# Optimization experiments

Measured on AMD Instinct MI355X. Metric: run time of the kernel, lower is better.

## Reference

```python
import jax, jax.numpy as jnp
import numpy as np

N, E, IN_DIM, HID, EMB, HEADS, B = 50000, 800000, 32, 128, 64, 4, 8
C = HID // HEADS
NEG_SLOPE = 0.2
LN_EPS = 1e-5
L = 3


def setup_inputs() -> dict:
    key = jax.random.key(0)
    ks = jax.random.split(key, 24)
    s = 0.05
    inp = {
        'x': jax.random.normal(ks[0], (N, IN_DIM), jnp.float32),
        'edge_index': jax.random.randint(ks[1], (2, E), 0, N),
        'edge_attr': jax.random.normal(ks[2], (E, 1), jnp.float32),
        'batch': jnp.sort(jax.random.randint(ks[3], (N,), 0, B)),
        'W_in': jax.random.normal(ks[4], (IN_DIM, HID), jnp.float32) * s,
        'b_in': jnp.zeros((HID,), jnp.float32),
        'Wl': jax.random.normal(ks[5], (L, HID, HID), jnp.float32) * s,
        'bl': jnp.zeros((L, HID), jnp.float32),
        'Wr': jax.random.normal(ks[6], (L, HID, HID), jnp.float32) * s,
        'br': jnp.zeros((L, HID), jnp.float32),
        'We': jax.random.normal(ks[7], (L, 1, HID), jnp.float32) * s,
        'att': jax.random.normal(ks[8], (L, HEADS, C), jnp.float32) * s,
        'bc': jnp.zeros((L, HID), jnp.float32),
        'ln_g': jnp.ones((L, HID), jnp.float32),
        'ln_b': jnp.zeros((L, HID), jnp.float32),
        'Wn': jax.random.normal(ks[9], (HID, EMB), jnp.float32) * s,
        'bn': jnp.zeros((EMB,), jnp.float32),
        'Wg1': jax.random.normal(ks[10], (HID, HID), jnp.float32) * s,
        'bg1': jnp.zeros((HID,), jnp.float32),
        'Wg2': jax.random.normal(ks[11], (HID, EMB), jnp.float32) * s,
        'bg2': jnp.zeros((EMB,), jnp.float32),
    }
    return inp


def _layernorm(x, g, b):
    mu = jnp.mean(x, axis=-1, keepdims=True)
    var = jnp.mean((x - mu) ** 2, axis=-1, keepdims=True)
    return (x - mu) * jax.lax.rsqrt(var + LN_EPS) * g + b


def reference(x, edge_index, edge_attr, batch, W_in, b_in, Wl, bl, Wr, br, We, att,
              bc, ln_g, ln_b, Wn, bn, Wg1, bg1, Wg2, bg2):
    src0, dst0 = edge_index[0], edge_index[1]
    # add self-loops; self-loop edge_attr = mean of incoming edge_attr (PyG fill_value='mean')
    ones = jnp.ones((E,), x.dtype)
    cnt = jax.ops.segment_sum(ones, dst0, num_segments=N)  # (N,)
    ea_self = jax.ops.segment_sum(edge_attr, dst0, num_segments=N) / jnp.maximum(cnt, 1.0)[:, None]
    ar = jnp.arange(N)
    src = jnp.concatenate([src0, ar])
    dst = jnp.concatenate([dst0, ar])
    ea = jnp.concatenate([edge_attr, ea_self], axis=0)  # (E+N, 1)

    h = x @ W_in + b_in  # (N, HID)
    for l in range(L):
        xl = (h @ Wl[l] + bl[l]).reshape(N, HEADS, C)   # source transform
        xr = (h @ Wr[l] + br[l]).reshape(N, HEADS, C)   # target transform
        ee = (ea @ We[l]).reshape(-1, HEADS, C)         # edge transform
        m = xl[src] + xr[dst] + ee                      # (E+N, H, C)
        m = jnp.where(m > 0, m, NEG_SLOPE * m)          # leaky_relu
        alpha = jnp.einsum('ehc,hc->eh', m, att[l])     # (E+N, H)
        amax = jax.ops.segment_max(alpha, dst, num_segments=N)
        ex = jnp.exp(alpha - amax[dst])
        den = jax.ops.segment_sum(ex, dst, num_segments=N)
        a = ex / den[dst]
        out = jax.ops.segment_sum(a[:, :, None] * xl[src], dst, num_segments=N)
        out = out.reshape(N, HID) + bc[l]
        h = _layernorm(h + jax.nn.elu(out), ln_g[l], ln_b[l])

    node_emb = h @ Wn + bn
    gsum = jax.ops.segment_sum(h, batch, num_segments=B)
    gcnt = jax.ops.segment_sum(jnp.ones((N, 1), h.dtype), batch, num_segments=B)
    gmean = gsum / jnp.maximum(gcnt, 1.0)
    graph_emb = jax.nn.elu(gmean @ Wg1 + bg1) @ Wg2 + bg2
    return node_emb, graph_emb, h
```

## Files before the change

kernel.cpp:

```cpp
#include <hip/hip_runtime.h>

#define NEG_SLOPE 0.2f
#define LN_EPS 1e-5f

typedef __attribute__((ext_vector_type(8))) short bf16x8;
typedef __attribute__((ext_vector_type(4))) float f32x4;

__device__ __forceinline__ ushort f2bf(float f) {
    uint u = __float_as_uint(f);
    u += 0x7fffu + ((u >> 16) & 1u);
    return (ushort)(u >> 16);
}


__global__ void count_kernel(const int* __restrict__ dst0, const float* __restrict__ eattr,
                             int* __restrict__ cnt, float* __restrict__ easum, int E_) {
    int e = blockIdx.x * 256 + threadIdx.x;
    if (e >= E_) return;
    int d = dst0[e];
    atomicAdd(&cnt[d], 1);
    atomicAdd(&easum[d], eattr[e]);
}

__global__ __launch_bounds__(256) void scan1_kernel(const int* __restrict__ cnt,
                                                    int* __restrict__ blocksum, int N_) {
    __shared__ int lds[256];
    int t = threadIdx.x;
    int i0 = blockIdx.x * 1024 + t * 4;
    int s = 0;
    if (i0 + 3 < N_) {
        int4 c4 = *(const int4*)(cnt + i0);
        s = c4.x + c4.y + c4.z + c4.w + 4;
    } else {
#pragma unroll
        for (int j = 0; j < 4; ++j)
            if (i0 + j < N_) s += cnt[i0 + j] + 1;
    }
    lds[t] = s;
    __syncthreads();
#pragma unroll
    for (int off = 128; off > 0; off >>= 1) {
        if (t < off) lds[t] += lds[t + off];
        __syncthreads();
    }
    if (t == 0) blocksum[blockIdx.x] = lds[0];
}

__global__ __launch_bounds__(1024) void scan2_kernel(const int* __restrict__ blocksum,
                                                     int* __restrict__ blockbase, int nb,
                                                     int* __restrict__ rowstart, int N_) {
    __shared__ int lds[1024];
    int t = threadIdx.x;
    int v = (t < nb) ? blocksum[t] : 0;
    lds[t] = v;
    __syncthreads();
    for (int off = 1; off < 1024; off <<= 1) {
        int u = (t >= off) ? lds[t - off] : 0;
        __syncthreads();
        lds[t] += u;
        __syncthreads();
    }
    if (t < nb) blockbase[t] = lds[t] - v;
    if (t == 0) rowstart[N_] = lds[nb - 1];
}

__global__ __launch_bounds__(256) void scan3_kernel(const int* __restrict__ cnt,
                                                    const float* __restrict__ easum,
                                                    const int* __restrict__ blockbase,
                                                    int* __restrict__ rowstart,
                                                    int2* __restrict__ csr,
                                                    int* __restrict__ cursor, int N_) {
    __shared__ int lds[256];
    int t = threadIdx.x;
    int i0 = blockIdx.x * 1024 + t * 4;
    int c[4];
    int nv = 0;
    int s = 0;
#pragma unroll
    for (int j = 0; j < 4; ++j) {
        if (i0 + j < N_) { c[j] = cnt[i0 + j]; s += c[j] + 1; nv = j + 1; }
        else c[j] = 0;
    }
    lds[t] = s;
    __syncthreads();
    for (int off = 1; off < 256; off <<= 1) {
        int u = (t >= off) ? lds[t - off] : 0;
        __syncthreads();
        lds[t] += u;
        __syncthreads();
    }
    int run = blockbase[blockIdx.x] + lds[t] - s;
#pragma unroll
    for (int j = 0; j < 4; ++j) {
        if (j < nv) {
            int i = i0 + j;
            rowstart[i] = run;
            int cc = c[j];
            csr[run] = make_int2(i, __float_as_int(easum[i] / (float)(cc > 1 ? cc : 1)));
            cursor[i] = run + 1;
            run += cc + 1;
        }
    }
}

__global__ void scatter_kernel(const int* __restrict__ src0, const int* __restrict__ dst0,
                               const float* __restrict__ eattr, int* __restrict__ cursor,
                               int2* __restrict__ csr, int E_) {
    int e = blockIdx.x * 256 + threadIdx.x;
    if (e >= E_) return;
    int d = dst0[e];
    int p = atomicAdd(&cursor[d], 1);
    csr[p] = make_int2(src0[e], __float_as_int(eattr[e]));
}

__global__ void pack_cvt_kernel(const float* __restrict__ Wl, const float* __restrict__ Wr,
                                const float* __restrict__ Win, const float* __restrict__ Wn,
                                const float* __restrict__ x, ushort* __restrict__ wpack,
                                ushort* __restrict__ xb, int nx4) {
    int idx = blockIdx.x * 256 + threadIdx.x;
    if (idx < 110592) {
        const float* src; int Ncol, rel;
        if (idx < 98304) {
            int m = idx >> 14; rel = idx & 16383;
            src = m < 3 ? Wl + m * 16384 : Wr + (m - 3) * 16384;
            Ncol = 128;
        } else if (idx < 102400) {
            rel = idx - 98304; src = Win; Ncol = 128;
        } else {
            rel = idx - 102400; src = Wn; Ncol = 64;
        }
        int j = rel & 7, lane = (rel >> 3) & 63, rest = rel >> 9;
        int nc16 = Ncol >> 4;
        int c = rest % nc16, ks = rest / nc16;
        int k = ks * 32 + ((lane >> 4) << 3) + j;
        int col = c * 16 + (lane & 15);
        wpack[idx] = f2bf(src[k * Ncol + col]);
    } else {
        int i = idx - 110592;
        if (i < nx4) {
            float4 v = *(const float4*)(x + (size_t)i * 4);
            ushort4 o;
            o.x = f2bf(v.x); o.y = f2bf(v.y); o.z = f2bf(v.z); o.w = f2bf(v.w);
            *(ushort4*)(xb + (size_t)i * 4) = o;
        }
    }
}


__global__ __launch_bounds__(256) void mfma_inproj(
    const ushort* __restrict__ x_bf, const ushort* __restrict__ Wp,
    const float* __restrict__ b_in, float* __restrict__ h, ushort* __restrict__ h_bf, int N_) {
    int wave = threadIdx.x >> 6, lane = threadIdx.x & 63;
    int row0 = blockIdx.x * 64 + wave * 16;
    int arow = row0 + (lane & 15); if (arow >= N_) arow = N_ - 1;
    int koff = (lane >> 4) * 8;
    bf16x8 a = *(const bf16x8*)(x_bf + (size_t)arow * 32 + koff);
    f32x4 acc[8];
#pragma unroll
    for (int c = 0; c < 8; ++c) acc[c] = {0.f, 0.f, 0.f, 0.f};
#pragma unroll
    for (int c = 0; c < 8; ++c) {
        bf16x8 b = *(const bf16x8*)(Wp + ((size_t)c * 64 + lane) * 8);
        acc[c] = __builtin_amdgcn_mfma_f32_16x16x32_bf16(a, b, acc[c], 0, 0, 0);
    }
    int srow = row0 + (lane >> 4) * 4;
    int scol = lane & 15;
#pragma unroll
    for (int c = 0; c < 8; ++c) {
        float bi = b_in[c * 16 + scol];
#pragma unroll
        for (int r = 0; r < 4; ++r) {
            int row = srow + r;
            if (row < N_) {
                float v = acc[c][r] + bi;
                h[(size_t)row * 128 + c * 16 + scol] = v;
                h_bf[(size_t)row * 128 + c * 16 + scol] = f2bf(v);
            }
        }
    }
}

__global__ __launch_bounds__(256, 1) void mfma_proj(
    const ushort* __restrict__ h_bf, const ushort* __restrict__ Wlp,
    const ushort* __restrict__ Wrp, const float* __restrict__ bl, const float* __restrict__ br,
    ushort* __restrict__ xl, ushort* __restrict__ xr, int N_) {
    int wave = threadIdx.x >> 6, lane = threadIdx.x & 63;
    int row0 = blockIdx.x * 128 + wave * 32;
    int ar0 = row0 + (lane & 15); if (ar0 >= N_) ar0 = N_ - 1;
    int ar1 = row0 + 16 + (lane & 15); if (ar1 >= N_) ar1 = N_ - 1;
    int koff = (lane >> 4) * 8;
    f32x4 accL[2][8], accR[2][8];
#pragma unroll
    for (int g = 0; g < 2; ++g)
#pragma unroll
        for (int c = 0; c < 8; ++c) { accL[g][c] = {0.f, 0.f, 0.f, 0.f}; accR[g][c] = {0.f, 0.f, 0.f, 0.f}; }
#pragma unroll
    for (int ks = 0; ks < 4; ++ks) {
        bf16x8 a0 = *(const bf16x8*)(h_bf + (size_t)ar0 * 128 + ks * 32 + koff);
        bf16x8 a1 = *(const bf16x8*)(h_bf + (size_t)ar1 * 128 + ks * 32 + koff);
        const ushort* wl = Wlp + ((size_t)ks * 8 * 64 + lane) * 8;
        const ushort* wr = Wrp + ((size_t)ks * 8 * 64 + lane) * 8;
#pragma unroll
        for (int c = 0; c < 8; ++c) {
            bf16x8 bL = *(const bf16x8*)(wl + c * 512);
            accL[0][c] = __builtin_amdgcn_mfma_f32_16x16x32_bf16(a0, bL, accL[0][c], 0, 0, 0);
            accL[1][c] = __builtin_amdgcn_mfma_f32_16x16x32_bf16(a1, bL, accL[1][c], 0, 0, 0);
            bf16x8 bR = *(const bf16x8*)(wr + c * 512);
            accR[0][c] = __builtin_amdgcn_mfma_f32_16x16x32_bf16(a0, bR, accR[0][c], 0, 0, 0);
            accR[1][c] = __builtin_amdgcn_mfma_f32_16x16x32_bf16(a1, bR, accR[1][c], 0, 0, 0);
        }
    }
    int scol = lane & 15;
#pragma unroll
    for (int g = 0; g < 2; ++g) {
        int srow = row0 + g * 16 + (lane >> 4) * 4;
#pragma unroll
        for (int c = 0; c < 8; ++c) {
            float bLv = bl[c * 16 + scol];
            float bRv = br[c * 16 + scol];
#pragma unroll
            for (int r = 0; r < 4; ++r) {
                int row = srow + r;
                if (row < N_) {
                    xl[(size_t)row * 128 + c * 16 + scol] = f2bf(accL[g][c][r] + bLv);
                    xr[(size_t)row * 128 + c * 16 + scol] = f2bf(accR[g][c][r] + bRv);
                }
            }
        }
    }
}

__global__ __launch_bounds__(256) void mfma_nodeemb(
    const ushort* __restrict__ h_bf, const ushort* __restrict__ Wp,
    const float* __restrict__ bn, float* __restrict__ node_emb, int N_) {
    int wave = threadIdx.x >> 6, lane = threadIdx.x & 63;
    int row0 = blockIdx.x * 64 + wave * 16;
    int arow = row0 + (lane & 15); if (arow >= N_) arow = N_ - 1;
    int koff = (lane >> 4) * 8;
    f32x4 acc[4];
#pragma unroll
    for (int c = 0; c < 4; ++c) acc[c] = {0.f, 0.f, 0.f, 0.f};
#pragma unroll
    for (int ks = 0; ks < 4; ++ks) {
        bf16x8 a = *(const bf16x8*)(h_bf + (size_t)arow * 128 + ks * 32 + koff);
#pragma unroll
        for (int c = 0; c < 4; ++c) {
            bf16x8 b = *(const bf16x8*)(Wp + ((size_t)(ks * 4 + c) * 64 + lane) * 8);
            acc[c] = __builtin_amdgcn_mfma_f32_16x16x32_bf16(a, b, acc[c], 0, 0, 0);
        }
    }
    int srow = row0 + (lane >> 4) * 4;
    int scol = lane & 15;
#pragma unroll
    for (int c = 0; c < 4; ++c) {
        float bi = bn[c * 16 + scol];
#pragma unroll
        for (int r = 0; r < 4; ++r) {
            int row = srow + r;
            if (row < N_) node_emb[(size_t)row * 64 + c * 16 + scol] = acc[c][r] + bi;
        }
    }
}


__device__ __forceinline__ float head16_sum(float x) {
    int v;
    v = __builtin_amdgcn_update_dpp(0, __float_as_int(x), 0xB1, 0xF, 0xF, true);
    x += __int_as_float(v);
    v = __builtin_amdgcn_update_dpp(0, __float_as_int(x), 0x4E, 0xF, 0xF, true);
    x += __int_as_float(v);
    v = __builtin_amdgcn_update_dpp(0, __float_as_int(x), 0x141, 0xF, 0xF, true);
    x += __int_as_float(v);
    v = __builtin_amdgcn_update_dpp(0, __float_as_int(x), 0x140, 0xF, 0xF, true);
    x += __int_as_float(v);
    return x;
}

__device__ __forceinline__ void edge_step(const uint* __restrict__ xlw,
                                          const int2* __restrict__ csr, int p, uint lane,
                                          float we2x, float we2y, float xr2x, float xr2y,
                                          float atx, float aty,
                                          float& d, float& ax, float& ay) {
    int2 e = csr[p];
    uint off = ((uint)e.x << 6) + lane;
    uint va = xlw[off];
    float xax = __uint_as_float(va << 16);
    float xay = __uint_as_float(va & 0xffff0000u);
    float ea = __int_as_float(e.y);
    float mx = xax + fmaf(ea, we2x, xr2x);
    float my = xay + fmaf(ea, we2y, xr2y);
    mx = fmaxf(mx, NEG_SLOPE * mx);
    my = fmaxf(my, NEG_SLOPE * my);
    float al = head16_sum(fmaf(my, aty, mx * atx));
    al = fminf(fmaxf(al, -60.f), 60.f);
    float pe = __expf(al);
    d += pe;
    ax = fmaf(pe, xax, ax);
    ay = fmaf(pe, xay, ay);
}

__global__ __launch_bounds__(256) void aggregate_kernel(
    float* __restrict__ h, const ushort* __restrict__ xl, const ushort* __restrict__ xr,
    const int* __restrict__ rowstart, const int2* __restrict__ csr,
    const float* __restrict__ We, const float* __restrict__ att, const float* __restrict__ bc,
    const float* __restrict__ ln_g, const float* __restrict__ ln_b,
    ushort* __restrict__ h_bf, float* __restrict__ h_out, int N_) {
    int wave = threadIdx.x >> 6;
    uint lane = threadIdx.x & 63;
    int n = blockIdx.x * 4 + wave;
    if (n >= N_) return;
    int c0 = lane * 2;
    int head = lane >> 4;
    const uint* xlw = (const uint*)xl;
    uint vr = *(const uint*)(xr + (size_t)n * 128 + c0);
    float xr2x = __uint_as_float(vr << 16);
    float xr2y = __uint_as_float(vr & 0xffff0000u);
    float2 we2 = *(const float2*)(We + c0);
    float2 at2 = *(const float2*)(att + head * 32 + (c0 & 31));
    int rs = rowstart[n], re = rowstart[n + 1];
    float d0 = 0.f, ax0 = 0.f, ay0 = 0.f;
    float d1 = 0.f, ax1 = 0.f, ay1 = 0.f;
    float d2 = 0.f, ax2 = 0.f, ay2 = 0.f;
    float d3 = 0.f, ax3 = 0.f, ay3 = 0.f;
    int p = rs;
    for (; p + 4 <= re; p += 4) {
        edge_step(xlw, csr, p,     lane, we2.x, we2.y, xr2x, xr2y, at2.x, at2.y, d0, ax0, ay0);
        edge_step(xlw, csr, p + 1, lane, we2.x, we2.y, xr2x, xr2y, at2.x, at2.y, d1, ax1, ay1);
        edge_step(xlw, csr, p + 2, lane, we2.x, we2.y, xr2x, xr2y, at2.x, at2.y, d2, ax2, ay2);
        edge_step(xlw, csr, p + 3, lane, we2.x, we2.y, xr2x, xr2y, at2.x, at2.y, d3, ax3, ay3);
    }
    for (; p < re; ++p)
        edge_step(xlw, csr, p, lane, we2.x, we2.y, xr2x, xr2y, at2.x, at2.y, d0, ax0, ay0);
    float den = (d0 + d1) + (d2 + d3);
    float accx = (ax0 + ax1) + (ax2 + ax3);
    float accy = (ay0 + ay1) + (ay2 + ay3);
    float inv = 1.f / den;
    float2 bc2 = *(const float2*)(bc + c0);
    float ox = accx * inv + bc2.x;
    float oy = accy * inv + bc2.y;
    ox = ox > 0.f ? ox : (__expf(ox) - 1.f);
    oy = oy > 0.f ? oy : (__expf(oy) - 1.f);
    float2 h2 = *(const float2*)(h + (size_t)n * 128 + c0);
    float tx = h2.x + ox, ty = h2.y + oy;
    float s1v = tx + ty;
    float s2v = tx * tx + ty * ty;
#pragma unroll
    for (int m = 1; m < 64; m <<= 1) {
        s1v += __shfl_xor(s1v, m);
        s2v += __shfl_xor(s2v, m);
    }
    float mu = s1v * (1.f / 128.f);
    float var = s2v * (1.f / 128.f) - mu * mu;
    float rstd = rsqrtf(var + LN_EPS);
    float2 g2 = *(const float2*)(ln_g + c0);
    float2 b2 = *(const float2*)(ln_b + c0);
    float2 hn;
    hn.x = (tx - mu) * rstd * g2.x + b2.x;
    hn.y = (ty - mu) * rstd * g2.y + b2.y;
    *(float2*)(h + (size_t)n * 128 + c0) = hn;
    uint packed = (uint)f2bf(hn.x) | ((uint)f2bf(hn.y) << 16);
    *(uint*)(h_bf + (size_t)n * 128 + c0) = packed;
    if (h_out) *(float2*)(h_out + (size_t)n * 128 + c0) = hn;
}


__global__ __launch_bounds__(256) void batch_kernel(
    const float* __restrict__ h, const int* __restrict__ batch,
    float* __restrict__ gsum, float* __restrict__ gcnt, int N_, int chunk) {
    int wave_id = (blockIdx.x * 256 + threadIdx.x) >> 6;
    int lane = threadIdx.x & 63;
    int w0 = wave_id * chunk;
    if (w0 >= N_) return;
    int w1 = w0 + chunk; if (w1 > N_) w1 = N_;
    int c0 = lane * 2;
    int cur_b = batch[w0];
    float accx = 0.f, accy = 0.f, cntf = 0.f;
    for (int n = w0; n < w1; ++n) {
        float2 h2 = *(const float2*)(h + (size_t)n * 128 + c0);
        int b = batch[n];
        if (b != cur_b) {
            atomicAdd(&gsum[cur_b * 128 + c0], accx);
            atomicAdd(&gsum[cur_b * 128 + c0 + 1], accy);
            if (lane == 0) atomicAdd(gcnt + cur_b, cntf);
            accx = accy = cntf = 0.f;
            cur_b = b;
        }
        accx += h2.x; accy += h2.y; cntf += 1.f;
    }
    atomicAdd(&gsum[cur_b * 128 + c0], accx);
    atomicAdd(&gsum[cur_b * 128 + c0 + 1], accy);
    if (lane == 0) atomicAdd(gcnt + cur_b, cntf);
}

__global__ void graph_kernel(const float* __restrict__ gsum, const float* __restrict__ gcnt,
                             const float* __restrict__ Wg1, const float* __restrict__ bg1,
                             const float* __restrict__ Wg2, const float* __restrict__ bg2,
                             float* __restrict__ graph_emb) {
    __shared__ float gm[8 * 128];
    __shared__ float t1[8 * 128];
    int t = threadIdx.x;
    for (int i = t; i < 1024; i += 256) {
        int b = i >> 7;
        float c = gcnt[b];
        c = c > 1.f ? c : 1.f;
        gm[i] = gsum[i] / c;
    }
    __syncthreads();
    for (int i = t; i < 1024; i += 256) {
        int r = i >> 7, j = i & 127;
        float acc = bg1[j];
        for (int k = 0; k < 128; ++k) acc += gm[r * 128 + k] * Wg1[k * 128 + j];
        t1[i] = acc > 0.f ? acc : (__expf(acc) - 1.f);
    }
    __syncthreads();
    for (int i = t; i < 512; i += 256) {
        int r = i >> 6, j = i & 63;
        float acc = bg2[j];
        for (int k = 0; k < 128; ++k) acc += t1[r * 128 + k] * Wg2[k * 64 + j];
        graph_emb[r * 64 + j] = acc;
    }
}


extern "C" void kernel_launch(void* const* d_in, const int* in_sizes, int n_in,
                              void* d_out, int out_size, void* d_ws, size_t ws_size,
                              hipStream_t stream) {
    const float* x         = (const float*)d_in[0];
    const int*   edge_index= (const int*)d_in[1];
    const float* edge_attr = (const float*)d_in[2];
    const int*   batch     = (const int*)d_in[3];
    const float* W_in      = (const float*)d_in[4];
    const float* b_in      = (const float*)d_in[5];
    const float* Wl        = (const float*)d_in[6];
    const float* bl        = (const float*)d_in[7];
    const float* Wr        = (const float*)d_in[8];
    const float* br        = (const float*)d_in[9];
    const float* We        = (const float*)d_in[10];
    const float* att       = (const float*)d_in[11];
    const float* bc        = (const float*)d_in[12];
    const float* ln_g      = (const float*)d_in[13];
    const float* ln_b      = (const float*)d_in[14];
    const float* Wn        = (const float*)d_in[15];
    const float* bn        = (const float*)d_in[16];
    const float* Wg1       = (const float*)d_in[17];
    const float* bg1       = (const float*)d_in[18];
    const float* Wg2       = (const float*)d_in[19];
    const float* bg2       = (const float*)d_in[20];

    const int N_ = in_sizes[3];
    const int E_ = in_sizes[2];

    const int* src0 = edge_index;
    const int* dst0 = edge_index + E_;

    float* ws = (float*)d_ws;
    float* h      = ws;
    float* gsum   = h + (size_t)N_ * 128;
    float* gcnt   = gsum + 1024;
    float* easum  = gcnt + 16;
    int* cnt      = (int*)(easum + N_);
    int* rowstart = cnt + N_;
    int* cursor   = rowstart + N_ + 2;
    int* blocksum = cursor + N_;
    int* blockbase= blocksum + 1024;
    int2* csr     = (int2*)(blockbase + 1024);
    ushort* h_bf  = (ushort*)(csr + (size_t)(E_ + N_));
    ushort* x_bf  = h_bf + (size_t)N_ * 128;
    ushort* xl_bf = x_bf + (size_t)N_ * 32;
    ushort* xr_bf = xl_bf + (size_t)N_ * 128;
    ushort* wpack = xr_bf + (size_t)N_ * 128;

    float* out_f     = (float*)d_out;
    float* node_emb  = out_f;
    float* graph_emb = out_f + (size_t)N_ * 64;
    float* h_out     = out_f + (size_t)N_ * 64 + 8 * 64;

    hipMemsetAsync(gsum, 0, (1024 + 16 + 2 * (size_t)N_) * sizeof(float), stream);

    int nx4 = N_ * 8;
    pack_cvt_kernel<<<(110592 + nx4 + 255) / 256, 256, 0, stream>>>(
        Wl, Wr, W_in, Wn, x, wpack, x_bf, nx4);
    count_kernel<<<(E_ + 255) / 256, 256, 0, stream>>>(dst0, edge_attr, cnt, easum, E_);

    int nb = (N_ + 1023) / 1024;
    scan1_kernel<<<nb, 256, 0, stream>>>(cnt, blocksum, N_);
    scan2_kernel<<<1, 1024, 0, stream>>>(blocksum, blockbase, nb, rowstart, N_);
    scan3_kernel<<<nb, 256, 0, stream>>>(cnt, easum, blockbase, rowstart, csr, cursor, N_);

    scatter_kernel<<<(E_ + 255) / 256, 256, 0, stream>>>(src0, dst0, edge_attr, cursor,
                                                         csr, E_);

    mfma_inproj<<<(N_ + 63) / 64, 256, 0, stream>>>(x_bf, wpack + 98304, b_in, h, h_bf, N_);

    for (int l = 0; l < 3; ++l) {
        mfma_proj<<<(N_ + 127) / 128, 256, 0, stream>>>(
            h_bf, wpack + l * 16384, wpack + (3 + l) * 16384,
            bl + l * 128, br + l * 128, xl_bf, xr_bf, N_);
        aggregate_kernel<<<(N_ + 3) / 4, 256, 0, stream>>>(
            h, xl_bf, xr_bf, rowstart, csr, We + l * 128, att + l * 128,
            bc + l * 128, ln_g + l * 128, ln_b + l * 128,
            h_bf, (l == 2) ? h_out : (float*)nullptr, N_);
    }

    mfma_nodeemb<<<(N_ + 63) / 64, 256, 0, stream>>>(h_bf, wpack + 102400, bn, node_emb, N_);
    {
        int total_waves = 2048;
        int chunk = (N_ + total_waves - 1) / total_waves;
        batch_kernel<<<total_waves / 4, 256, 0, stream>>>(h, batch, gsum, gcnt, N_, chunk);
    }
    graph_kernel<<<1, 256, 0, stream>>>(gsum, gcnt, Wg1, bg1, Wg2, bg2, graph_emb);
}
```

Measured before the change: 562.8 us.

## Build CSR with atomic ranks and compute self-loop means in a separate pass

The count kernel now records each edge's slot rank from the atomic counter and drops the float atomic that summed edge attributes. The scatter kernel places edges using that rank plus the row start, with no second atomic pass over a cursor array. A new self-loop kernel walks each row to compute the mean edge attribute for the self-loop entry. The trade is an extra rank array of E ints and one more kernel launch, in exchange for fewer atomics in CSR construction.

Result: faster. 499.7 us (-11.2%).

```diff
diff --git a/kernel.cpp b/kernel.cpp
--- a/kernel.cpp
+++ b/kernel.cpp
@@ -13,13 +13,11 @@
 }
 
 
-__global__ void count_kernel(const int* __restrict__ dst0, const float* __restrict__ eattr,
-                             int* __restrict__ cnt, float* __restrict__ easum, int E_) {
+__global__ void count_kernel(const int* __restrict__ dst0, int* __restrict__ cnt,
+                             int* __restrict__ rank, int E_) {
     int e = blockIdx.x * 256 + threadIdx.x;
     if (e >= E_) return;
-    int d = dst0[e];
-    atomicAdd(&cnt[d], 1);
-    atomicAdd(&easum[d], eattr[e]);
+    rank[e] = atomicAdd(&cnt[dst0[e]], 1);
 }
 
 __global__ __launch_bounds__(256) void scan1_kernel(const int* __restrict__ cnt,
@@ -65,11 +63,8 @@
 }
 
 __global__ __launch_bounds__(256) void scan3_kernel(const int* __restrict__ cnt,
-                                                    const float* __restrict__ easum,
                                                     const int* __restrict__ blockbase,
-                                                    int* __restrict__ rowstart,
-                                                    int2* __restrict__ csr,
-                                                    int* __restrict__ cursor, int N_) {
+                                                    int* __restrict__ rowstart, int N_) {
     __shared__ int lds[256];
     int t = threadIdx.x;
     int i0 = blockIdx.x * 1024 + t * 4;
@@ -93,24 +88,31 @@
 #pragma unroll
     for (int j = 0; j < 4; ++j) {
         if (j < nv) {
-            int i = i0 + j;
-            rowstart[i] = run;
-            int cc = c[j];
-            csr[run] = make_int2(i, __float_as_int(easum[i] / (float)(cc > 1 ? cc : 1)));
-            cursor[i] = run + 1;
-            run += cc + 1;
+            rowstart[i0 + j] = run;
+            run += c[j] + 1;
         }
     }
 }
 
 __global__ void scatter_kernel(const int* __restrict__ src0, const int* __restrict__ dst0,
-                               const float* __restrict__ eattr, int* __restrict__ cursor,
-                               int2* __restrict__ csr, int E_) {
+                               const float* __restrict__ eattr, const int* __restrict__ rank,
+                               const int* __restrict__ rowstart, int2* __restrict__ csr, int E_) {
     int e = blockIdx.x * 256 + threadIdx.x;
     if (e >= E_) return;
     int d = dst0[e];
-    int p = atomicAdd(&cursor[d], 1);
+    int p = rowstart[d] + 1 + rank[e];
     csr[p] = make_int2(src0[e], __float_as_int(eattr[e]));
+}
+
+__global__ void selfloop_kernel(const int* __restrict__ rowstart, int2* __restrict__ csr,
+                                int N_) {
+    int n = blockIdx.x * 256 + threadIdx.x;
+    if (n >= N_) return;
+    int rs = rowstart[n], re = rowstart[n + 1];
+    float s = 0.f;
+    for (int p = rs + 1; p < re; ++p) s += __int_as_float(csr[p].y);
+    int c = re - rs - 1;
+    csr[rs] = make_int2(n, __float_as_int(s / (float)(c > 1 ? c : 1)));
 }
 
 __global__ void pack_cvt_kernel(const float* __restrict__ Wl, const float* __restrict__ Wr,
@@ -457,11 +459,10 @@
     float* h      = ws;
     float* gsum   = h + (size_t)N_ * 128;
     float* gcnt   = gsum + 1024;
-    float* easum  = gcnt + 16;
-    int* cnt      = (int*)(easum + N_);
+    int* cnt      = (int*)(gcnt + 16);
     int* rowstart = cnt + N_;
-    int* cursor   = rowstart + N_ + 2;
-    int* blocksum = cursor + N_;
+    int* rank     = rowstart + N_ + 2;
+    int* blocksum = rank + E_;
     int* blockbase= blocksum + 1024;
     int2* csr     = (int2*)(blockbase + 1024);
     ushort* h_bf  = (ushort*)(csr + (size_t)(E_ + N_));
@@ -475,20 +476,21 @@
     float* graph_emb = out_f + (size_t)N_ * 64;
     float* h_out     = out_f + (size_t)N_ * 64 + 8 * 64;
 
-    hipMemsetAsync(gsum, 0, (1024 + 16 + 2 * (size_t)N_) * sizeof(float), stream);
+    hipMemsetAsync(gsum, 0, (1024 + 16 + (size_t)N_) * sizeof(float), stream);
 
     int nx4 = N_ * 8;
     pack_cvt_kernel<<<(110592 + nx4 + 255) / 256, 256, 0, stream>>>(
         Wl, Wr, W_in, Wn, x, wpack, x_bf, nx4);
-    count_kernel<<<(E_ + 255) / 256, 256, 0, stream>>>(dst0, edge_attr, cnt, easum, E_);
+    count_kernel<<<(E_ + 255) / 256, 256, 0, stream>>>(dst0, cnt, rank, E_);
 
     int nb = (N_ + 1023) / 1024;
     scan1_kernel<<<nb, 256, 0, stream>>>(cnt, blocksum, N_);
     scan2_kernel<<<1, 1024, 0, stream>>>(blocksum, blockbase, nb, rowstart, N_);
-    scan3_kernel<<<nb, 256, 0, stream>>>(cnt, easum, blockbase, rowstart, csr, cursor, N_);
-
-    scatter_kernel<<<(E_ + 255) / 256, 256, 0, stream>>>(src0, dst0, edge_attr, cursor,
-                                                         csr, E_);
+    scan3_kernel<<<nb, 256, 0, stream>>>(cnt, blockbase, rowstart, N_);
+
+    scatter_kernel<<<(E_ + 255) / 256, 256, 0, stream>>>(src0, dst0, edge_attr, rank,
+                                                         rowstart, csr, E_);
+    selfloop_kernel<<<(N_ + 255) / 256, 256, 0, stream>>>(rowstart, csr, N_);
 
     mfma_inproj<<<(N_ + 63) / 64, 256, 0, stream>>>(x_bf, wpack + 98304, b_in, h, h_bf, N_);
 
```
